# Kernel tuning notes

Hardware: AMD Instinct MI355X
Metric: run time of the kernel (lower is better)

Reference implementation:

```python
import jax, jax.numpy as jnp
import numpy as np

N = 16384          # num_nodes
B = 2              # batch_size
F = 32             # feature_size (hard-coded in module)
G = 16             # num_gru_units
OUT = 16           # output_dim


def _normalized_laplacian(adj):
    # calculate_laplacian_with_self_loop: D^-1/2 (A + I) D^-1/2
    a = adj + jnp.eye(adj.shape[0], dtype=adj.dtype)
    d = a.sum(axis=1)
    dinv = jax.lax.rsqrt(d)
    return dinv[:, None] * a * dinv[None, :]


def setup_inputs() -> dict:
    key = jax.random.key(0)
    k1, k2, k3, k4 = jax.random.split(key, 4)
    adj = (jax.random.uniform(k1, (N, N), dtype=jnp.float32) < 0.01).astype(jnp.float32)
    laplacian = _normalized_laplacian(adj)
    inputs = jax.random.normal(k2, (B, N, F), dtype=jnp.float32)
    hidden_state = jax.random.normal(k3, (B, N * G), dtype=jnp.float32)
    # xavier_uniform for weights [(G+F), OUT]
    limit = np.sqrt(6.0 / (G + F + OUT)).astype(np.float32)
    weights = jax.random.uniform(k4, (G + F, OUT), dtype=jnp.float32, minval=-limit, maxval=limit)
    biases = jnp.zeros((OUT,), dtype=jnp.float32)
    return {"inputs": inputs, "hidden_state": hidden_state, "laplacian": laplacian,
            "weights": weights, "biases": biases}


def reference(inputs, hidden_state, laplacian, weights, biases):
    b, n, f = inputs.shape
    g = weights.shape[0] - f
    out_dim = weights.shape[1]
    h = hidden_state.reshape(b, n, g)
    cat = jnp.concatenate([inputs, h], axis=2)              # [B, N, F+G]
    # laplacian @ concat over the node dimension (same math as the
    # reshape/transpose dance + per-batch sparse GEMM loop in the original)
    ax = jnp.einsum('mn,bnc->bmc', laplacian, cat)          # [B, N, F+G]
    out = ax @ weights + biases                             # [B, N, OUT]
    return out.reshape(b, n * out_dim)
```

## Files before the change

kernel.cpp:

```cpp
#include <hip/hip_runtime.h>
#include <hip/hip_bf16.h>


#define NN   16384
#define FF   32
#define GG   16
#define OUTD 16
#define C96  96
#define BM   64
#define BK   64
#define SPLITK 4
#define KCHUNK (NN / SPLITK)
#define KITERS (KCHUNK / BK)

typedef __attribute__((ext_vector_type(8))) short short8;
typedef __attribute__((ext_vector_type(4))) float f32x4;

using as1_void = __attribute__((address_space(1))) void;
using as3_void = __attribute__((address_space(3))) void;

__device__ __forceinline__ unsigned short f2bf(float f) {
  __hip_bfloat16 h = __float2bfloat16(f);
  return __builtin_bit_cast(unsigned short, h);
}

__global__ __launch_bounds__(256) void prep_xt(const float* __restrict__ inp,
                                               const float* __restrict__ hid,
                                               unsigned short* __restrict__ xt) {
  __shared__ float lds_cat[C96][64];
  const int tid = threadIdx.x;
  const int n0 = blockIdx.x * 64;

#pragma unroll
  for (int r = 0; r < 2; ++r) {
    int fi = tid + r * 256;
    int n = fi >> 3;
    int f4 = fi & 7;
#pragma unroll
    for (int b = 0; b < 2; ++b) {
      const float4* src = (const float4*)(inp + ((size_t)b * NN + (n0 + n)) * FF) + f4;
      float4 v = *src;
      int c = b * 48 + f4 * 4;
      lds_cat[c + 0][n] = v.x;
      lds_cat[c + 1][n] = v.y;
      lds_cat[c + 2][n] = v.z;
      lds_cat[c + 3][n] = v.w;
    }
  }
  {
    int n = tid >> 2;
    int g4 = tid & 3;
#pragma unroll
    for (int b = 0; b < 2; ++b) {
      const float4* src = (const float4*)(hid + ((size_t)b * NN + (n0 + n)) * GG) + g4;
      float4 v = *src;
      int c = b * 48 + 32 + g4 * 4;
      lds_cat[c + 0][n] = v.x;
      lds_cat[c + 1][n] = v.y;
      lds_cat[c + 2][n] = v.z;
      lds_cat[c + 3][n] = v.w;
    }
  }
  __syncthreads();
#pragma unroll
  for (int r = 0; r < 3; ++r) {
    int u = tid + r * 256;
    int c = u >> 3;
    int nn = (u & 7) * 8;
    short8 o;
#pragma unroll
    for (int j = 0; j < 8; ++j) o[j] = (short)f2bf(lds_cat[c][nn + j]);
    *(short8*)(xt + (size_t)c * NN + n0 + nn) = o;
  }
}

__global__ __launch_bounds__(256, 4) void spmm_main(const float* __restrict__ L,
                                                    const unsigned short* __restrict__ xt,
                                                    float* __restrict__ cp) {
  __shared__ __align__(16) float lds_a[BM * BK];
  __shared__ __align__(16) unsigned short lds_b[C96 * BK];

  const int tid = threadIdx.x;
  const int wave = tid >> 6;
  const int lane = tid & 63;
  const int m0 = blockIdx.x * BM;
  const int kbase = blockIdx.y * KCHUNK;

  const float* asrc[4];
  float* adst[4];
#pragma unroll
  for (int a = 0; a < 4; ++a) {
    int s = wave * 256 + a * 64 + lane;
    int row = s >> 4;
    int cu = (s & 15) ^ (row & 15);
    asrc[a] = L + (size_t)(m0 + row) * NN + kbase + cu * 4;
    adst[a] = lds_a + (wave * 256 + a * 64) * 4;
  }
  const unsigned short* bsrc[3];
  unsigned short* bdst[3];
#pragma unroll
  for (int bi = 0; bi < 3; ++bi) {
    int s = wave * 192 + bi * 64 + lane;
    int c = s >> 3;
    int kg = (s & 7) ^ (c & 7);
    bsrc[bi] = xt + (size_t)c * NN + kbase + kg * 8;
    bdst[bi] = lds_b + (wave * 192 + bi * 64) * 8;
  }

  const int rowA = wave * 16 + (lane & 15);
  const int lq = lane >> 4;
  int aoff[2][2];
#pragma unroll
  for (int kk = 0; kk < 2; ++kk) {
    int cu0 = kk * 8 + lq * 2;
    aoff[kk][0] = (rowA * 16 + (cu0 ^ (rowA & 15))) * 4;
    aoff[kk][1] = (rowA * 16 + ((cu0 + 1) ^ (rowA & 15))) * 4;
  }
  int boff[2][6];
#pragma unroll
  for (int kk = 0; kk < 2; ++kk)
#pragma unroll
    for (int t = 0; t < 6; ++t) {
      int c = t * 16 + (lane & 15);
      int kg = kk * 4 + lq;
      boff[kk][t] = (c * 8 + (kg ^ (c & 7))) * 8;
    }

  f32x4 acc[6];
#pragma unroll
  for (int t = 0; t < 6; ++t) acc[t] = (f32x4){0.f, 0.f, 0.f, 0.f};

  for (int it = 0; it < KITERS; ++it) {
    const int ko = it * BK;
#pragma unroll
    for (int a = 0; a < 4; ++a)
      __builtin_amdgcn_global_load_lds((const as1_void*)(asrc[a] + ko),
                                       (as3_void*)adst[a], 16, 0, 0);
#pragma unroll
    for (int bi = 0; bi < 3; ++bi)
      __builtin_amdgcn_global_load_lds((const as1_void*)(bsrc[bi] + ko),
                                       (as3_void*)bdst[bi], 16, 0, 0);
    __syncthreads();

#pragma unroll
    for (int kk = 0; kk < 2; ++kk) {
      f32x4 a0 = *(const f32x4*)(lds_a + aoff[kk][0]);
      f32x4 a1 = *(const f32x4*)(lds_a + aoff[kk][1]);
      short8 af;
      af[0] = (short)f2bf(a0[0]);
      af[1] = (short)f2bf(a0[1]);
      af[2] = (short)f2bf(a0[2]);
      af[3] = (short)f2bf(a0[3]);
      af[4] = (short)f2bf(a1[0]);
      af[5] = (short)f2bf(a1[1]);
      af[6] = (short)f2bf(a1[2]);
      af[7] = (short)f2bf(a1[3]);
#pragma unroll
      for (int t = 0; t < 6; ++t) {
        short8 bf = *(const short8*)(lds_b + boff[kk][t]);
        acc[t] = __builtin_amdgcn_mfma_f32_16x16x32_bf16(af, bf, acc[t], 0, 0, 0);
      }
    }
    __syncthreads();
  }

  float* cpd = cp + ((size_t)blockIdx.y * NN + m0) * C96;
#pragma unroll
  for (int t = 0; t < 6; ++t) {
    int col = t * 16 + (lane & 15);
#pragma unroll
    for (int r = 0; r < 4; ++r) {
      int row = wave * 16 + lq * 4 + r;
      cpd[(size_t)row * C96 + col] = acc[t][r];
    }
  }
}

__global__ __launch_bounds__(256) void epilogue(const float* __restrict__ cp,
                                                const float* __restrict__ w,
                                                const float* __restrict__ bias,
                                                float* __restrict__ out) {
  __shared__ float lds_c[64 * 97];
  __shared__ float lds_w[48 * 16];
  __shared__ float lds_bias[16];
  const int tid = threadIdx.x;
  const int n0 = blockIdx.x * 64;

  for (int i = tid; i < 768; i += 256) lds_w[i] = w[i];
  if (tid < 16) lds_bias[tid] = bias[tid];

  const size_t base = (size_t)n0 * C96;
#pragma unroll
  for (int i = 0; i < 24; ++i) {
    int e = tid + i * 256;
    float s = 0.f;
#pragma unroll
    for (int sp = 0; sp < 4; ++sp)
      s += cp[(size_t)sp * (NN * C96) + base + e];
    lds_c[e + e / 96] = s;
  }
  __syncthreads();

  const int node = tid >> 2;
  const int b = (tid >> 1) & 1;
  const int o0 = (tid & 1) * 8;
  const float* crow = &lds_c[node * 97 + b * 48];
  float accv[8];
#pragma unroll
  for (int o = 0; o < 8; ++o) accv[o] = lds_bias[o0 + o];
#pragma unroll
  for (int j = 0; j < 48; ++j) {
    float cv = crow[j];
#pragma unroll
    for (int o = 0; o < 8; ++o) accv[o] += cv * lds_w[j * 16 + o0 + o];
  }
  size_t ob = (size_t)b * (NN * OUTD) + (size_t)(n0 + node) * OUTD + o0;
  float4 v0 = {accv[0], accv[1], accv[2], accv[3]};
  float4 v1 = {accv[4], accv[5], accv[6], accv[7]};
  *(float4*)(out + ob) = v0;
  *(float4*)(out + ob + 4) = v1;
}

extern "C" void kernel_launch(void* const* d_in, const int* in_sizes, int n_in,
                              void* d_out, int out_size, void* d_ws, size_t ws_size,
                              hipStream_t stream) {
  (void)in_sizes; (void)n_in; (void)out_size; (void)ws_size;
  const float* inp = (const float*)d_in[0];
  const float* hid = (const float*)d_in[1];
  const float* lap = (const float*)d_in[2];
  const float* wts = (const float*)d_in[3];
  const float* bia = (const float*)d_in[4];
  float* out = (float*)d_out;

  unsigned short* xt = (unsigned short*)d_ws;
  float* cp = (float*)((char*)d_ws + (4u << 20));

  prep_xt<<<NN / 64, 256, 0, stream>>>(inp, hid, xt);
  spmm_main<<<dim3(NN / BM, SPLITK), 256, 0, stream>>>(lap, xt, cp);
  epilogue<<<NN / 64, 256, 0, stream>>>(cp, wts, bia, out);
}
```

Baseline: 1.345 ms.

## Load GEMM operands straight to registers with prefetch, drop LDS staging

The split-K dense GEMM kernel no longer stages tiles through LDS. Each wave now loads its two 16-row A fragments and six B fragments directly from global memory into registers, with one-iteration software prefetch. Each wave covers 32 rows, and blocks start their K loop at a staggered phase so they do not all hit the same columns at once. This removes LDS traffic and block barriers, but B fragments are no longer shared between waves through LDS, so more global/L2 loads are issued and register pressure rises.

```diff
diff --git a/kernel.cpp b/kernel.cpp
--- a/kernel.cpp
+++ b/kernel.cpp
@@ -7,17 +7,12 @@
 #define GG   16
 #define OUTD 16
 #define C96  96
-#define BM   64
-#define BK   64
 #define SPLITK 4
 #define KCHUNK (NN / SPLITK)
-#define KITERS (KCHUNK / BK)
+#define KIT    (KCHUNK / 32)
 
 typedef __attribute__((ext_vector_type(8))) short short8;
 typedef __attribute__((ext_vector_type(4))) float f32x4;
-
-using as1_void = __attribute__((address_space(1))) void;
-using as3_void = __attribute__((address_space(3))) void;
 
 __device__ __forceinline__ unsigned short f2bf(float f) {
   __hip_bfloat16 h = __float2bfloat16(f);
@@ -74,106 +69,86 @@
   }
 }
 
-__global__ __launch_bounds__(256, 4) void spmm_main(const float* __restrict__ L,
-                                                    const unsigned short* __restrict__ xt,
-                                                    float* __restrict__ cp) {
-  __shared__ __align__(16) float lds_a[BM * BK];
-  __shared__ __align__(16) unsigned short lds_b[C96 * BK];
-
+__global__ __launch_bounds__(256) void spmm_main(const float* __restrict__ L,
+                                                 const unsigned short* __restrict__ xt,
+                                                 float* __restrict__ cp) {
   const int tid = threadIdx.x;
   const int wave = tid >> 6;
   const int lane = tid & 63;
-  const int m0 = blockIdx.x * BM;
-  const int kbase = blockIdx.y * KCHUNK;
-
-  const float* asrc[4];
-  float* adst[4];
-#pragma unroll
-  for (int a = 0; a < 4; ++a) {
-    int s = wave * 256 + a * 64 + lane;
-    int row = s >> 4;
-    int cu = (s & 15) ^ (row & 15);
-    asrc[a] = L + (size_t)(m0 + row) * NN + kbase + cu * 4;
-    adst[a] = lds_a + (wave * 256 + a * 64) * 4;
-  }
-  const unsigned short* bsrc[3];
-  unsigned short* bdst[3];
-#pragma unroll
-  for (int bi = 0; bi < 3; ++bi) {
-    int s = wave * 192 + bi * 64 + lane;
-    int c = s >> 3;
-    int kg = (s & 7) ^ (c & 7);
-    bsrc[bi] = xt + (size_t)c * NN + kbase + kg * 8;
-    bdst[bi] = lds_b + (wave * 192 + bi * 64) * 8;
-  }
-
-  const int rowA = wave * 16 + (lane & 15);
-  const int lq = lane >> 4;
-  int aoff[2][2];
-#pragma unroll
-  for (int kk = 0; kk < 2; ++kk) {
-    int cu0 = kk * 8 + lq * 2;
-    aoff[kk][0] = (rowA * 16 + (cu0 ^ (rowA & 15))) * 4;
-    aoff[kk][1] = (rowA * 16 + ((cu0 + 1) ^ (rowA & 15))) * 4;
-  }
-  int boff[2][6];
-#pragma unroll
-  for (int kk = 0; kk < 2; ++kk)
+  const int m = lane & 15;
+  const int quad = lane >> 4;
+  const int bx = blockIdx.x;
+  const int sp = bx & 3;
+  const int rg = bx >> 2;
+  const int m0 = rg * 128 + wave * 32;
+  const int kb = sp * KCHUNK;
+  const int phase = (rg * 29) & (KIT - 1);
+
+  const float* arow0 = L + (size_t)(m0 + m) * NN + kb + quad * 8;
+  const float* arow1 = arow0 + (size_t)16 * NN;
+  const unsigned short* brow[6];
+#pragma unroll
+  for (int t = 0; t < 6; ++t)
+    brow[t] = xt + (size_t)(t * 16 + m) * NN + kb + quad * 8;
+
+  f32x4 acc[2][6];
+#pragma unroll
+  for (int i = 0; i < 2; ++i)
+#pragma unroll
+    for (int t = 0; t < 6; ++t) acc[i][t] = (f32x4){0.f, 0.f, 0.f, 0.f};
+
+  int k0 = phase * 32;
+  float4 a0n = *(const float4*)(arow0 + k0);
+  float4 a1n = *(const float4*)(arow0 + k0 + 4);
+  float4 a2n = *(const float4*)(arow1 + k0);
+  float4 a3n = *(const float4*)(arow1 + k0 + 4);
+  short8 bn[6];
+#pragma unroll
+  for (int t = 0; t < 6; ++t) bn[t] = *(const short8*)(brow[t] + k0);
+
+  for (int it = 0; it < KIT; ++it) {
+    float4 a0 = a0n, a1 = a1n, a2 = a2n, a3 = a3n;
+    short8 bc[6];
+#pragma unroll
+    for (int t = 0; t < 6; ++t) bc[t] = bn[t];
+
+    int kn = ((it + 1 + phase) & (KIT - 1)) * 32;
+    a0n = *(const float4*)(arow0 + kn);
+    a1n = *(const float4*)(arow0 + kn + 4);
+    a2n = *(const float4*)(arow1 + kn);
+    a3n = *(const float4*)(arow1 + kn + 4);
+#pragma unroll
+    for (int t = 0; t < 6; ++t) bn[t] = *(const short8*)(brow[t] + kn);
+
+    short8 af0, af1;
+    af0[0] = (short)f2bf(a0.x); af0[1] = (short)f2bf(a0.y);
+    af0[2] = (short)f2bf(a0.z); af0[3] = (short)f2bf(a0.w);
+    af0[4] = (short)f2bf(a1.x); af0[5] = (short)f2bf(a1.y);
+    af0[6] = (short)f2bf(a1.z); af0[7] = (short)f2bf(a1.w);
+    af1[0] = (short)f2bf(a2.x); af1[1] = (short)f2bf(a2.y);
+    af1[2] = (short)f2bf(a2.z); af1[3] = (short)f2bf(a2.w);
+    af1[4] = (short)f2bf(a3.x); af1[5] = (short)f2bf(a3.y);
+    af1[6] = (short)f2bf(a3.z); af1[7] = (short)f2bf(a3.w);
+
 #pragma unroll
     for (int t = 0; t < 6; ++t) {
-      int c = t * 16 + (lane & 15);
-      int kg = kk * 4 + lq;
-      boff[kk][t] = (c * 8 + (kg ^ (c & 7))) * 8;
-    }
-
-  f32x4 acc[6];
-#pragma unroll
-  for (int t = 0; t < 6; ++t) acc[t] = (f32x4){0.f, 0.f, 0.f, 0.f};
-
-  for (int it = 0; it < KITERS; ++it) {
-    const int ko = it * BK;
-#pragma unroll
-    for (int a = 0; a < 4; ++a)
-      __builtin_amdgcn_global_load_lds((const as1_void*)(asrc[a] + ko),
-                                       (as3_void*)adst[a], 16, 0, 0);
-#pragma unroll
-    for (int bi = 0; bi < 3; ++bi)
-      __builtin_amdgcn_global_load_lds((const as1_void*)(bsrc[bi] + ko),
-                                       (as3_void*)bdst[bi], 16, 0, 0);
-    __syncthreads();
-
-#pragma unroll
-    for (int kk = 0; kk < 2; ++kk) {
-      f32x4 a0 = *(const f32x4*)(lds_a + aoff[kk][0]);
-      f32x4 a1 = *(const f32x4*)(lds_a + aoff[kk][1]);
-      short8 af;
-      af[0] = (short)f2bf(a0[0]);
-      af[1] = (short)f2bf(a0[1]);
-      af[2] = (short)f2bf(a0[2]);
-      af[3] = (short)f2bf(a0[3]);
-      af[4] = (short)f2bf(a1[0]);
-      af[5] = (short)f2bf(a1[1]);
-      af[6] = (short)f2bf(a1[2]);
-      af[7] = (short)f2bf(a1[3]);
-#pragma unroll
-      for (int t = 0; t < 6; ++t) {
-        short8 bf = *(const short8*)(lds_b + boff[kk][t]);
-        acc[t] = __builtin_amdgcn_mfma_f32_16x16x32_bf16(af, bf, acc[t], 0, 0, 0);
+      acc[0][t] = __builtin_amdgcn_mfma_f32_16x16x32_bf16(af0, bc[t], acc[0][t], 0, 0, 0);
+      acc[1][t] = __builtin_amdgcn_mfma_f32_16x16x32_bf16(af1, bc[t], acc[1][t], 0, 0, 0);
+    }
+  }
+
+  float* cpd = cp + ((size_t)sp * NN + m0) * C96;
+#pragma unroll
+  for (int tile = 0; tile < 2; ++tile)
+#pragma unroll
+    for (int t = 0; t < 6; ++t) {
+      int col = t * 16 + m;
+#pragma unroll
+      for (int r = 0; r < 4; ++r) {
+        int row = tile * 16 + quad * 4 + r;
+        cpd[(size_t)row * C96 + col] = acc[tile][t][r];
       }
     }
-    __syncthreads();
-  }
-
-  float* cpd = cp + ((size_t)blockIdx.y * NN + m0) * C96;
-#pragma unroll
-  for (int t = 0; t < 6; ++t) {
-    int col = t * 16 + (lane & 15);
-#pragma unroll
-    for (int r = 0; r < 4; ++r) {
-      int row = wave * 16 + lq * 4 + r;
-      cpd[(size_t)row * C96 + col] = acc[t][r];
-    }
-  }
 }
 
 __global__ __launch_bounds__(256) void epilogue(const float* __restrict__ cp,
@@ -195,8 +170,8 @@
     int e = tid + i * 256;
     float s = 0.f;
 #pragma unroll
-    for (int sp = 0; sp < 4; ++sp)
-      s += cp[(size_t)sp * (NN * C96) + base + e];
+    for (int sp = 0; sp < SPLITK; ++sp)
+      s += cp[(size_t)sp * ((size_t)NN * C96) + base + e];
     lds_c[e + e / 96] = s;
   }
   __syncthreads();
@@ -214,7 +189,7 @@
 #pragma unroll
     for (int o = 0; o < 8; ++o) accv[o] += cv * lds_w[j * 16 + o0 + o];
   }
-  size_t ob = (size_t)b * (NN * OUTD) + (size_t)(n0 + node) * OUTD + o0;
+  size_t ob = (size_t)b * ((size_t)NN * OUTD) + (size_t)(n0 + node) * OUTD + o0;
   float4 v0 = {accv[0], accv[1], accv[2], accv[3]};
   float4 v1 = {accv[4], accv[5], accv[6], accv[7]};
   *(float4*)(out + ob) = v0;
@@ -236,6 +211,6 @@
   float* cp = (float*)((char*)d_ws + (4u << 20));
 
   prep_xt<<<NN / 64, 256, 0, stream>>>(inp, hid, xt);
-  spmm_main<<<dim3(NN / BM, SPLITK), 256, 0, stream>>>(lap, xt, cp);
+  spmm_main<<<NN / 128 * SPLITK, 256, 0, stream>>>(lap, xt, cp);
   epilogue<<<NN / 64, 256, 0, stream>>>(cp, wts, bia, out);
 }
```

Result: slower. 1.443 ms (+7.3%).
